# Optimization experiments

Measured on AMD Instinct MI355X. Metric: run time of the kernel, lower is better.

## Reference

```python
import jax, jax.numpy as jnp
import numpy as np

N = 8192
QS = 128
KS = 128
F = 256
EPS = 1e-5     # BatchNorm1d default eps
SLOPE = 0.01   # LeakyReLU default negative_slope


def _leaky(x):
    return jnp.where(x >= 0, x, SLOPE * x)


def _mlp_bn(x, w1, b1, w2, b2, gamma, beta):
    # Sequential(Linear, LeakyReLU, Linear, LeakyReLU) then BatchNorm1d (training mode)
    h = _leaky(x @ w1 + b1)
    h = _leaky(h @ w2 + b2)
    mean = h.mean(axis=0)
    var = h.var(axis=0)  # biased variance, as torch BN uses for normalization
    return gamma * (h - mean) * jax.lax.rsqrt(var + EPS) + beta


def setup_inputs() -> dict:
    key = jax.random.key(0)
    ks = jax.random.split(key, 24)

    def lin_w(k_, fi, fo):
        s = 1.0 / np.sqrt(fi)
        return jax.random.uniform(k_, (fi, fo), minval=-s, maxval=s, dtype=jnp.float32)

    def lin_b(k_, fi, fo):
        s = 1.0 / np.sqrt(fi)
        return jax.random.uniform(k_, (fo,), minval=-s, maxval=s, dtype=jnp.float32)

    A = (jax.random.uniform(ks[0], (N, N)) < 0.004).astype(jnp.float32)
    q = jax.random.normal(ks[1], (N, QS), dtype=jnp.float32)
    k = jax.random.normal(ks[2], (N, KS), dtype=jnp.float32)

    inp = {"A": A, "q": q, "k": k}
    i = 3
    for pre, fi in (("q", QS), ("k", KS), ("v", KS)):
        inp[pre + "_w1"] = lin_w(ks[i], fi, F); i += 1
        inp[pre + "_b1"] = lin_b(ks[i], fi, F); i += 1
        inp[pre + "_w2"] = lin_w(ks[i], F, F); i += 1
        inp[pre + "_b2"] = lin_b(ks[i], F, F); i += 1
        inp[pre + "_gamma"] = jnp.ones((F,), jnp.float32)
        inp[pre + "_beta"] = jnp.zeros((F,), jnp.float32)
    return inp


def reference(A, q, k,
              q_w1, q_b1, q_w2, q_b2, q_gamma, q_beta,
              k_w1, k_b1, k_w2, k_b2, k_gamma, k_beta,
              v_w1, v_b1, v_w2, v_b2, v_gamma, v_beta):
    qe1 = _mlp_bn(q, q_w1, q_b1, q_w2, q_b2, q_gamma, q_beta)   # [N, F]
    ke1 = _mlp_bn(k, k_w1, k_b1, k_w2, k_b2, k_gamma, k_beta)   # [N, F]
    prod = (qe1 @ ke1.T) / jnp.sqrt(jnp.float32(F))             # [N, N]
    # NOTE: faithful to source — mask zeroes scores (not -inf) before softmax
    masked = A * prod
    attn = jax.nn.softmax(masked, axis=1)
    ve1 = _mlp_bn(k, v_w1, v_b1, v_w2, v_b2, v_gamma, v_beta)   # [N, F]
    return attn @ ve1                                            # [N, F]
```

## Files before the change

kernel.cpp:

```cpp
#include <hip/hip_runtime.h>

#define NROWS 8192
#define FDIM 256
#define CAP 128

typedef _Float16 half8_t __attribute__((ext_vector_type(8)));
typedef _Float16 half4_t __attribute__((ext_vector_type(4)));
typedef float floatx4 __attribute__((ext_vector_type(4)));

struct MlpPtrs {
  const float* w1[3]; const float* b1[3];
  const float* w2[3]; const float* b2[3];
  const float* gamma[3]; const float* beta[3];
};

__global__ __launch_bounds__(256) void prep_kernel(
    MlpPtrs p, _Float16* __restrict__ w1p, _Float16* __restrict__ w2p) {
  int task = blockIdx.y;
  int tid = blockIdx.x * 256 + threadIdx.x;
  int m = task % 3;
  bool isw2 = task >= 3;
  int K = isw2 ? 256 : 128;
  if (tid >= K * 256) return;
  const float* src = isw2 ? p.w2[m] : p.w1[m];
  _Float16* dst = isw2 ? (w2p + m * 65536) : (w1p + m * 32768);
  int j = tid & 7, lane = (tid >> 3) & 63, rest = tid >> 9;
  int ktiles = K >> 5;
  int k_tile = rest % ktiles, n_tile = rest / ktiles;
  int kk = k_tile * 32 + (lane >> 4) * 8 + j;
  int nn = n_tile * 16 + (lane & 15);
  dst[tid] = (_Float16)src[kk * 256 + nn];
}

__global__ __launch_bounds__(256) void gemm1_kernel(
    const float* __restrict__ q, const float* __restrict__ k,
    const _Float16* __restrict__ w1p, MlpPtrs p, _Float16* __restrict__ h1) {
  const int mlp = blockIdx.z;
  const float* X = (mlp == 0) ? q : k;
  const _Float16* wp = w1p + mlp * 32768;
  _Float16* out = h1 + (size_t)mlp * (NROWS * FDIM);
  const float* bias = p.b1[mlp];
  int lane = threadIdx.x & 63, wave = threadIdx.x >> 6;
  int lm = lane & 15, lq = lane >> 4;
  int m0 = blockIdx.x * 64 + wave * 16;
  int n0 = blockIdx.y * 64;
  floatx4 acc[4];
  #pragma unroll
  for (int t = 0; t < 4; ++t) acc[t] = (floatx4){0.f, 0.f, 0.f, 0.f};
  const float* ap = X + (size_t)(m0 + lm) * 128 + lq * 8;
  const half8_t* wp8 = (const half8_t*)wp;
  #pragma unroll
  for (int kt = 0; kt < 4; ++kt) {
    floatx4 a0 = *(const floatx4*)(ap + kt * 32);
    floatx4 a1 = *(const floatx4*)(ap + kt * 32 + 4);
    half8_t a = (half8_t){(_Float16)a0[0], (_Float16)a0[1], (_Float16)a0[2], (_Float16)a0[3],
                          (_Float16)a1[0], (_Float16)a1[1], (_Float16)a1[2], (_Float16)a1[3]};
    #pragma unroll
    for (int t = 0; t < 4; ++t) {
      half8_t b = wp8[(((n0 >> 4) + t) * 4 + kt) * 64 + lane];
      acc[t] = __builtin_amdgcn_mfma_f32_16x16x32_f16(a, b, acc[t], 0, 0, 0);
    }
  }
  #pragma unroll
  for (int t = 0; t < 4; ++t) {
    int col = n0 + t * 16 + lm;
    float bb = bias[col];
    #pragma unroll
    for (int r = 0; r < 4; ++r) {
      float v = acc[t][r] + bb;
      v = (v >= 0.f) ? v : 0.01f * v;
      out[(size_t)(m0 + lq * 4 + r) * FDIM + col] = (_Float16)v;
    }
  }
}

__global__ __launch_bounds__(256) void gemm2_kernel(
    const _Float16* __restrict__ h1, const _Float16* __restrict__ w2p,
    MlpPtrs p, _Float16* __restrict__ e1,
    float* __restrict__ colsum, float* __restrict__ colsumsq) {
  const int mlp = blockIdx.z;
  const _Float16* X = h1 + (size_t)mlp * (NROWS * FDIM);
  const _Float16* wp = w2p + mlp * 65536;
  _Float16* out = e1 + (size_t)mlp * (NROWS * FDIM);
  const float* bias = p.b2[mlp];
  int lane = threadIdx.x & 63, wave = threadIdx.x >> 6;
  int lm = lane & 15, lq = lane >> 4;
  int m0 = blockIdx.x * 64 + wave * 16;
  int n0 = blockIdx.y * 64;
  floatx4 acc[4];
  #pragma unroll
  for (int t = 0; t < 4; ++t) acc[t] = (floatx4){0.f, 0.f, 0.f, 0.f};
  const half8_t* ap = (const half8_t*)(X + (size_t)(m0 + lm) * 256 + lq * 8);
  const half8_t* wp8 = (const half8_t*)wp;
  #pragma unroll
  for (int kt = 0; kt < 8; ++kt) {
    half8_t a = ap[kt * 4];
    #pragma unroll
    for (int t = 0; t < 4; ++t) {
      half8_t b = wp8[(((n0 >> 4) + t) * 8 + kt) * 64 + lane];
      acc[t] = __builtin_amdgcn_mfma_f32_16x16x32_f16(a, b, acc[t], 0, 0, 0);
    }
  }
  #pragma unroll
  for (int t = 0; t < 4; ++t) {
    int col = n0 + t * 16 + lm;
    float bb = bias[col];
    float s = 0.f, s2 = 0.f;
    #pragma unroll
    for (int r = 0; r < 4; ++r) {
      float v = acc[t][r] + bb;
      v = (v >= 0.f) ? v : 0.01f * v;
      out[(size_t)(m0 + lq * 4 + r) * FDIM + col] = (_Float16)v;
      s += v; s2 += v * v;
    }
    s  += __shfl_xor(s, 16, 64);  s  += __shfl_xor(s, 32, 64);
    s2 += __shfl_xor(s2, 16, 64); s2 += __shfl_xor(s2, 32, 64);
    if (lq == 0) {
      atomicAdd(&colsum[mlp * FDIM + col], s);
      atomicAdd(&colsumsq[mlp * FDIM + col], s2);
    }
  }
}

__global__ __launch_bounds__(256) void stats_kernel(
    const float* __restrict__ colsum, const float* __restrict__ colsumsq,
    MlpPtrs p, float* __restrict__ scaleA, float* __restrict__ shiftA) {
  int c = threadIdx.x;
  #pragma unroll
  for (int m = 0; m < 3; ++m) {
    float mean = colsum[m * FDIM + c] * (1.f / NROWS);
    float var = colsumsq[m * FDIM + c] * (1.f / NROWS) - mean * mean;
    float sc = p.gamma[m][c] * rsqrtf(var + 1e-5f);
    scaleA[m * FDIM + c] = sc;
    shiftA[m * FDIM + c] = p.beta[m][c] - mean * sc;
  }
}

__global__ __launch_bounds__(256) void attn_kernel(
    const float* __restrict__ A, const _Float16* __restrict__ e1,
    const float* __restrict__ scaleA, const float* __restrict__ shiftA,
    const float* __restrict__ colsum, float* __restrict__ out) {
  const _Float16* qe = e1;
  const _Float16* ke = e1 + (size_t)1 * NROWS * FDIM;
  const _Float16* ve = e1 + (size_t)2 * NROWS * FDIM;
  int lane = threadIdx.x & 63, wave = threadIdx.x >> 6;
  int i = blockIdx.x * 4 + wave;
  __shared__ int sj[4][CAP];
  __shared__ float sw[4][CAP];
  __shared__ int cnt[4];
  if (lane == 0) cnt[wave] = 0;

  const floatx4* row = (const floatx4*)(A + (size_t)i * NROWS);
  for (int b = 0; b < 4; ++b) {
    floatx4 av[8];
    #pragma unroll
    for (int it = 0; it < 8; ++it)
      av[it] = __builtin_nontemporal_load(&row[(b * 8 + it) * 64 + lane]);
    #pragma unroll
    for (int it = 0; it < 8; ++it) {
      int base = ((b * 8 + it) * 64 + lane) * 4;
      int cols[4]; int c = 0;
      if (av[it][0] != 0.f) cols[c++] = base + 0;
      if (av[it][1] != 0.f) cols[c++] = base + 1;
      if (av[it][2] != 0.f) cols[c++] = base + 2;
      if (av[it][3] != 0.f) cols[c++] = base + 3;
      if (c) {
        int pos = atomicAdd(&cnt[wave], c);
        for (int l = 0; l < c; ++l) if (pos + l < CAP) sj[wave][pos + l] = cols[l];
      }
    }
  }
  int nnz = cnt[wave] < CAP ? cnt[wave] : CAP;

  int cl = lane & 15, g = lane >> 4;
  const half8_t* qp = (const half8_t*)(qe + (size_t)i * FDIM + cl * 16);
  half8_t qa = qp[0], qb8 = qp[1];
  const floatx4* sq4 = (const floatx4*)(scaleA + cl * 16);
  const floatx4* hq4 = (const floatx4*)(shiftA + cl * 16);
  const floatx4* sk4 = (const floatx4*)(scaleA + FDIM + cl * 16);
  const floatx4* hk4 = (const floatx4*)(shiftA + FDIM + cl * 16);
  float qk[16]; float qb = 0.f;
  #pragma unroll
  for (int v4 = 0; v4 < 4; ++v4) {
    floatx4 sq = sq4[v4], hq = hq4[v4], sk = sk4[v4], hk = hk4[v4];
    #pragma unroll
    for (int r = 0; r < 4; ++r) {
      int c = v4 * 4 + r;
      float qr = (c < 8) ? (float)qa[c] : (float)qb8[c - 8];
      float qn = qr * sq[r] + hq[r];
      qk[c] = qn * sk[r] * 0.0625f;
      qb += qn * hk[r] * 0.0625f;
    }
  }

  for (int e = g; e < nnz; e += 4) {
    int j = sj[wave][e];
    const half8_t* kp = (const half8_t*)(ke + (size_t)j * FDIM + cl * 16);
    half8_t ka = kp[0], kb = kp[1];
    float s = qb;
    #pragma unroll
    for (int r = 0; r < 8; ++r)
      s += qk[r] * (float)ka[r] + qk[r + 8] * (float)kb[r];
    #pragma unroll
    for (int off = 8; off >= 1; off >>= 1) s += __shfl_xor(s, off, 64);
    if (cl == 0) sw[wave][e] = s;
  }

  float v0 = lane < nnz ? sw[wave][lane] : 0.f;
  float v1 = lane + 64 < nnz ? sw[wave][lane + 64] : 0.f;
  float m = fmaxf(fmaxf(v0, v1), 0.f);
  #pragma unroll
  for (int off = 32; off >= 1; off >>= 1) m = fmaxf(m, __shfl_xor(m, off, 64));
  float em = __expf(-m);
  float w0 = lane < nnz ? __expf(v0 - m) : 0.f;
  float w1 = lane + 64 < nnz ? __expf(v1 - m) : 0.f;
  float ls = w0 + w1;
  #pragma unroll
  for (int off = 32; off >= 1; off >>= 1) ls += __shfl_xor(ls, off, 64);
  if (lane < nnz) sw[wave][lane] = w0 - em;
  if (lane + 64 < nnz) sw[wave][lane + 64] = w1 - em;
  float wsum = ls - (float)nnz * em;
  float inv = 1.f / (ls + (float)(NROWS - nnz) * em);

  floatx4 acc = (floatx4){0.f, 0.f, 0.f, 0.f};
  for (int e = 0; e < nnz; ++e) {
    int j = sj[wave][e];
    float w = sw[wave][e];
    half4_t vv = *(const half4_t*)(ve + (size_t)j * FDIM + lane * 4);
    acc[0] += w * (float)vv[0]; acc[1] += w * (float)vv[1];
    acc[2] += w * (float)vv[2]; acc[3] += w * (float)vv[3];
  }

  floatx4 sv = *(const floatx4*)(scaleA + 2 * FDIM + lane * 4);
  floatx4 sh = *(const floatx4*)(shiftA + 2 * FDIM + lane * 4);
  floatx4 cs = *(const floatx4*)(colsum + 2 * FDIM + lane * 4);
  float bg = wsum + em * (float)NROWS;
  floatx4 o;
  #pragma unroll
  for (int r = 0; r < 4; ++r)
    o[r] = inv * (sv[r] * (acc[r] + em * cs[r]) + sh[r] * bg);
  __builtin_nontemporal_store(o, (floatx4*)(out + (size_t)i * FDIM + lane * 4));
}

extern "C" void kernel_launch(void* const* d_in, const int* in_sizes, int n_in,
                              void* d_out, int out_size, void* d_ws, size_t ws_size,
                              hipStream_t stream) {
  const float* A = (const float*)d_in[0];
  const float* q = (const float*)d_in[1];
  const float* k = (const float*)d_in[2];
  MlpPtrs p;
  for (int m = 0; m < 3; ++m) {
    const int b = 3 + m * 6;
    p.w1[m]    = (const float*)d_in[b + 0];
    p.b1[m]    = (const float*)d_in[b + 1];
    p.w2[m]    = (const float*)d_in[b + 2];
    p.b2[m]    = (const float*)d_in[b + 3];
    p.gamma[m] = (const float*)d_in[b + 4];
    p.beta[m]  = (const float*)d_in[b + 5];
  }
  char* ws = (char*)d_ws;
  const size_t MB = 1024 * 1024;
  _Float16* h1  = (_Float16*)(ws + 0);
  _Float16* e1  = (_Float16*)(ws + 12 * MB);
  _Float16* w1p = (_Float16*)(ws + 24 * MB);
  _Float16* w2p = (_Float16*)(ws + 24 * MB + 192 * 1024);
  float* colsum   = (float*)(ws + 25 * MB);
  float* colsumsq = colsum + 3 * FDIM;
  float* scaleA   = colsumsq + 3 * FDIM;
  float* shiftA   = scaleA + 3 * FDIM;

  (void)hipMemsetAsync(colsum, 0, 2 * 3 * FDIM * sizeof(float), stream);
  prep_kernel<<<dim3(256, 6, 1), 256, 0, stream>>>(p, w1p, w2p);
  gemm1_kernel<<<dim3(128, 4, 3), 256, 0, stream>>>(q, k, w1p, p, h1);
  gemm2_kernel<<<dim3(128, 4, 3), 256, 0, stream>>>(h1, w2p, p, e1, colsum, colsumsq);
  stats_kernel<<<1, 256, 0, stream>>>(colsum, colsumsq, p, scaleA, shiftA);
  attn_kernel<<<NROWS / 4, 256, 0, stream>>>(A, e1, scaleA, shiftA, colsum, (float*)d_out);
}
```

Measured before the change: 456.0 us.

## Cut launches: fold memset and stats into other kernels, widen GEMM tiles

Zeroing of the column-sum buffers moves into the weight-prep kernel, and the single-block stats kernel is removed; each attention block now computes BN scale and shift into shared memory itself. Both MLP GEMM kernels now compute all 256 output columns per block (16 accumulators) instead of 64, so each A row is loaded once and grid size drops fourfold. This removes two launches and their serialization, at the cost of redundant stats work in every attention block, more registers and fewer blocks in the GEMMs.

```diff
diff --git a/kernel.cpp b/kernel.cpp
--- a/kernel.cpp
+++ b/kernel.cpp
@@ -15,9 +15,11 @@
 };
 
 __global__ __launch_bounds__(256) void prep_kernel(
-    MlpPtrs p, _Float16* __restrict__ w1p, _Float16* __restrict__ w2p) {
+    MlpPtrs p, _Float16* __restrict__ w1p, _Float16* __restrict__ w2p,
+    float* __restrict__ colzero) {
   int task = blockIdx.y;
   int tid = blockIdx.x * 256 + threadIdx.x;
+  if (task == 0 && tid < 2 * 3 * FDIM) colzero[tid] = 0.f;
   int m = task % 3;
   bool isw2 = task >= 3;
   int K = isw2 ? 256 : 128;
@@ -43,10 +45,9 @@
   int lane = threadIdx.x & 63, wave = threadIdx.x >> 6;
   int lm = lane & 15, lq = lane >> 4;
   int m0 = blockIdx.x * 64 + wave * 16;
-  int n0 = blockIdx.y * 64;
-  floatx4 acc[4];
-  #pragma unroll
-  for (int t = 0; t < 4; ++t) acc[t] = (floatx4){0.f, 0.f, 0.f, 0.f};
+  floatx4 acc[16];
+  #pragma unroll
+  for (int t = 0; t < 16; ++t) acc[t] = (floatx4){0.f, 0.f, 0.f, 0.f};
   const float* ap = X + (size_t)(m0 + lm) * 128 + lq * 8;
   const half8_t* wp8 = (const half8_t*)wp;
   #pragma unroll
@@ -56,14 +57,14 @@
     half8_t a = (half8_t){(_Float16)a0[0], (_Float16)a0[1], (_Float16)a0[2], (_Float16)a0[3],
                           (_Float16)a1[0], (_Float16)a1[1], (_Float16)a1[2], (_Float16)a1[3]};
     #pragma unroll
-    for (int t = 0; t < 4; ++t) {
-      half8_t b = wp8[(((n0 >> 4) + t) * 4 + kt) * 64 + lane];
+    for (int t = 0; t < 16; ++t) {
+      half8_t b = wp8[(t * 4 + kt) * 64 + lane];
       acc[t] = __builtin_amdgcn_mfma_f32_16x16x32_f16(a, b, acc[t], 0, 0, 0);
     }
   }
   #pragma unroll
-  for (int t = 0; t < 4; ++t) {
-    int col = n0 + t * 16 + lm;
+  for (int t = 0; t < 16; ++t) {
+    int col = t * 16 + lm;
     float bb = bias[col];
     #pragma unroll
     for (int r = 0; r < 4; ++r) {
@@ -86,24 +87,23 @@
   int lane = threadIdx.x & 63, wave = threadIdx.x >> 6;
   int lm = lane & 15, lq = lane >> 4;
   int m0 = blockIdx.x * 64 + wave * 16;
-  int n0 = blockIdx.y * 64;
-  floatx4 acc[4];
-  #pragma unroll
-  for (int t = 0; t < 4; ++t) acc[t] = (floatx4){0.f, 0.f, 0.f, 0.f};
+  floatx4 acc[16];
+  #pragma unroll
+  for (int t = 0; t < 16; ++t) acc[t] = (floatx4){0.f, 0.f, 0.f, 0.f};
   const half8_t* ap = (const half8_t*)(X + (size_t)(m0 + lm) * 256 + lq * 8);
   const half8_t* wp8 = (const half8_t*)wp;
   #pragma unroll
   for (int kt = 0; kt < 8; ++kt) {
     half8_t a = ap[kt * 4];
     #pragma unroll
-    for (int t = 0; t < 4; ++t) {
-      half8_t b = wp8[(((n0 >> 4) + t) * 8 + kt) * 64 + lane];
+    for (int t = 0; t < 16; ++t) {
+      half8_t b = wp8[(t * 8 + kt) * 64 + lane];
       acc[t] = __builtin_amdgcn_mfma_f32_16x16x32_f16(a, b, acc[t], 0, 0, 0);
     }
   }
   #pragma unroll
-  for (int t = 0; t < 4; ++t) {
-    int col = n0 + t * 16 + lm;
+  for (int t = 0; t < 16; ++t) {
+    int col = t * 16 + lm;
     float bb = bias[col];
     float s = 0.f, s2 = 0.f;
     #pragma unroll
@@ -122,33 +122,33 @@
   }
 }
 
-__global__ __launch_bounds__(256) void stats_kernel(
-    const float* __restrict__ colsum, const float* __restrict__ colsumsq,
-    MlpPtrs p, float* __restrict__ scaleA, float* __restrict__ shiftA) {
-  int c = threadIdx.x;
-  #pragma unroll
-  for (int m = 0; m < 3; ++m) {
-    float mean = colsum[m * FDIM + c] * (1.f / NROWS);
-    float var = colsumsq[m * FDIM + c] * (1.f / NROWS) - mean * mean;
-    float sc = p.gamma[m][c] * rsqrtf(var + 1e-5f);
-    scaleA[m * FDIM + c] = sc;
-    shiftA[m * FDIM + c] = p.beta[m][c] - mean * sc;
-  }
-}
-
 __global__ __launch_bounds__(256) void attn_kernel(
     const float* __restrict__ A, const _Float16* __restrict__ e1,
-    const float* __restrict__ scaleA, const float* __restrict__ shiftA,
-    const float* __restrict__ colsum, float* __restrict__ out) {
+    const float* __restrict__ colsum, const float* __restrict__ colsumsq,
+    MlpPtrs p, float* __restrict__ out) {
   const _Float16* qe = e1;
   const _Float16* ke = e1 + (size_t)1 * NROWS * FDIM;
   const _Float16* ve = e1 + (size_t)2 * NROWS * FDIM;
-  int lane = threadIdx.x & 63, wave = threadIdx.x >> 6;
+  int tid = threadIdx.x, lane = tid & 63, wave = tid >> 6;
   int i = blockIdx.x * 4 + wave;
   __shared__ int sj[4][CAP];
   __shared__ float sw[4][CAP];
   __shared__ int cnt[4];
+  __shared__ float ls_scale[3 * FDIM], ls_shift[3 * FDIM];
+
+  {
+    int c = tid;
+    #pragma unroll
+    for (int m = 0; m < 3; ++m) {
+      float mean = colsum[m * FDIM + c] * (1.f / NROWS);
+      float var = colsumsq[m * FDIM + c] * (1.f / NROWS) - mean * mean;
+      float sc = p.gamma[m][c] * rsqrtf(var + 1e-5f);
+      ls_scale[m * FDIM + c] = sc;
+      ls_shift[m * FDIM + c] = p.beta[m][c] - mean * sc;
+    }
+  }
   if (lane == 0) cnt[wave] = 0;
+  __syncthreads();
 
   const floatx4* row = (const floatx4*)(A + (size_t)i * NROWS);
   for (int b = 0; b < 4; ++b) {
@@ -175,10 +175,10 @@
   int cl = lane & 15, g = lane >> 4;
   const half8_t* qp = (const half8_t*)(qe + (size_t)i * FDIM + cl * 16);
   half8_t qa = qp[0], qb8 = qp[1];
-  const floatx4* sq4 = (const floatx4*)(scaleA + cl * 16);
-  const floatx4* hq4 = (const floatx4*)(shiftA + cl * 16);
-  const floatx4* sk4 = (const floatx4*)(scaleA + FDIM + cl * 16);
-  const floatx4* hk4 = (const floatx4*)(shiftA + FDIM + cl * 16);
+  const floatx4* sq4 = (const floatx4*)(ls_scale + cl * 16);
+  const floatx4* hq4 = (const floatx4*)(ls_shift + cl * 16);
+  const floatx4* sk4 = (const floatx4*)(ls_scale + FDIM + cl * 16);
+  const floatx4* hk4 = (const floatx4*)(ls_shift + FDIM + cl * 16);
   float qk[16]; float qb = 0.f;
   #pragma unroll
   for (int v4 = 0; v4 < 4; ++v4) {
@@ -231,8 +231,8 @@
     acc[2] += w * (float)vv[2]; acc[3] += w * (float)vv[3];
   }
 
-  floatx4 sv = *(const floatx4*)(scaleA + 2 * FDIM + lane * 4);
-  floatx4 sh = *(const floatx4*)(shiftA + 2 * FDIM + lane * 4);
+  floatx4 sv = *(const floatx4*)(ls_scale + 2 * FDIM + lane * 4);
+  floatx4 sh = *(const floatx4*)(ls_shift + 2 * FDIM + lane * 4);
   floatx4 cs = *(const floatx4*)(colsum + 2 * FDIM + lane * 4);
   float bg = wsum + em * (float)NROWS;
   floatx4 o;
@@ -266,13 +266,9 @@
   _Float16* w2p = (_Float16*)(ws + 24 * MB + 192 * 1024);
   float* colsum   = (float*)(ws + 25 * MB);
   float* colsumsq = colsum + 3 * FDIM;
-  float* scaleA   = colsumsq + 3 * FDIM;
-  float* shiftA   = scaleA + 3 * FDIM;
-
-  (void)hipMemsetAsync(colsum, 0, 2 * 3 * FDIM * sizeof(float), stream);
-  prep_kernel<<<dim3(256, 6, 1), 256, 0, stream>>>(p, w1p, w2p);
-  gemm1_kernel<<<dim3(128, 4, 3), 256, 0, stream>>>(q, k, w1p, p, h1);
-  gemm2_kernel<<<dim3(128, 4, 3), 256, 0, stream>>>(h1, w2p, p, e1, colsum, colsumsq);
-  stats_kernel<<<1, 256, 0, stream>>>(colsum, colsumsq, p, scaleA, shiftA);
-  attn_kernel<<<NROWS / 4, 256, 0, stream>>>(A, e1, scaleA, shiftA, colsum, (float*)d_out);
-}
+
+  prep_kernel<<<dim3(256, 6, 1), 256, 0, stream>>>(p, w1p, w2p, colsum);
+  gemm1_kernel<<<dim3(128, 1, 3), 256, 0, stream>>>(q, k, w1p, p, h1);
+  gemm2_kernel<<<dim3(128, 1, 3), 256, 0, stream>>>(h1, w2p, p, e1, colsum, colsumsq);
+  attn_kernel<<<NROWS / 4, 256, 0, stream>>>(A, e1, colsum, colsumsq, p, (float*)d_out);
+}
```

New measurement: 487.1 us. 6.8% more time.

## Overlap adjacency scan with MLP GEMMs by folding row compaction into GEMM launches

Applied to the files above, without the earlier changes.

Moves the dense adjacency scan, which reads 256 MB and compacts each row into column indices, out of the attention kernel. The scan now runs as extra blocks inside the two GEMM kernels, half the rows in each, so its memory traffic overlaps the MFMA work. The attention kernel then reads only the compacted index lists. This adds a workspace round-trip for the indices and makes the GEMM launches mix memory-bound and compute-bound blocks.

```diff
diff --git a/kernel.cpp b/kernel.cpp
--- a/kernel.cpp
+++ b/kernel.cpp
@@ -13,6 +13,37 @@
   const float* w2[3]; const float* b2[3];
   const float* gamma[3]; const float* beta[3];
 };
+
+__device__ __forceinline__ void scan_row(
+    int r, int lane, int wave, const float* __restrict__ A,
+    int* __restrict__ colidx, int* __restrict__ rowcnt,
+    int (&sj)[4][CAP], int (&cnt)[4]) {
+  if (lane == 0) cnt[wave] = 0;
+  const floatx4* row = (const floatx4*)(A + (size_t)r * NROWS);
+  for (int b = 0; b < 4; ++b) {
+    floatx4 av[8];
+    #pragma unroll
+    for (int it = 0; it < 8; ++it)
+      av[it] = __builtin_nontemporal_load(&row[(b * 8 + it) * 64 + lane]);
+    #pragma unroll
+    for (int it = 0; it < 8; ++it) {
+      int base = ((b * 8 + it) * 64 + lane) * 4;
+      int cols[4]; int c = 0;
+      if (av[it][0] != 0.f) cols[c++] = base + 0;
+      if (av[it][1] != 0.f) cols[c++] = base + 1;
+      if (av[it][2] != 0.f) cols[c++] = base + 2;
+      if (av[it][3] != 0.f) cols[c++] = base + 3;
+      if (c) {
+        int pos = atomicAdd(&cnt[wave], c);
+        for (int l = 0; l < c; ++l) if (pos + l < CAP) sj[wave][pos + l] = cols[l];
+      }
+    }
+  }
+  int nnz = cnt[wave] < CAP ? cnt[wave] : CAP;
+  if (lane < nnz) colidx[(size_t)r * CAP + lane] = sj[wave][lane];
+  if (lane + 64 < nnz) colidx[(size_t)r * CAP + lane + 64] = sj[wave][lane + 64];
+  if (lane == 0) rowcnt[r] = nnz;
+}
 
 __global__ __launch_bounds__(256) void prep_kernel(
     MlpPtrs p, _Float16* __restrict__ w1p, _Float16* __restrict__ w2p) {
@@ -34,19 +65,28 @@
 
 __global__ __launch_bounds__(256) void gemm1_kernel(
     const float* __restrict__ q, const float* __restrict__ k,
-    const _Float16* __restrict__ w1p, MlpPtrs p, _Float16* __restrict__ h1) {
-  const int mlp = blockIdx.z;
-  const float* X = (mlp == 0) ? q : k;
-  const _Float16* wp = w1p + mlp * 32768;
-  _Float16* out = h1 + (size_t)mlp * (NROWS * FDIM);
-  const float* bias = p.b1[mlp];
+    const _Float16* __restrict__ w1p, MlpPtrs p, _Float16* __restrict__ h1,
+    const float* __restrict__ A, int* __restrict__ colidx, int* __restrict__ rowcnt) {
+  __shared__ int sj[4][CAP];
+  __shared__ int cnt[4];
   int lane = threadIdx.x & 63, wave = threadIdx.x >> 6;
+  int bid = blockIdx.x;
+  if (bid < 1024) {
+    scan_row(bid * 4 + wave, lane, wave, A, colidx, rowcnt, sj, cnt);
+    return;
+  }
+  int t = bid - 1024;
+  int z = t / 512, rem = t % 512, by = rem / 128, bx = rem % 128;
+  const float* X = (z == 0) ? q : k;
+  const _Float16* wp = w1p + z * 32768;
+  _Float16* out = h1 + (size_t)z * (NROWS * FDIM);
+  const float* bias = p.b1[z];
   int lm = lane & 15, lq = lane >> 4;
-  int m0 = blockIdx.x * 64 + wave * 16;
-  int n0 = blockIdx.y * 64;
+  int m0 = bx * 64 + wave * 16;
+  int n0 = by * 64;
   floatx4 acc[4];
   #pragma unroll
-  for (int t = 0; t < 4; ++t) acc[t] = (floatx4){0.f, 0.f, 0.f, 0.f};
+  for (int u = 0; u < 4; ++u) acc[u] = (floatx4){0.f, 0.f, 0.f, 0.f};
   const float* ap = X + (size_t)(m0 + lm) * 128 + lq * 8;
   const half8_t* wp8 = (const half8_t*)wp;
   #pragma unroll
@@ -56,18 +96,18 @@
     half8_t a = (half8_t){(_Float16)a0[0], (_Float16)a0[1], (_Float16)a0[2], (_Float16)a0[3],
                           (_Float16)a1[0], (_Float16)a1[1], (_Float16)a1[2], (_Float16)a1[3]};
     #pragma unroll
-    for (int t = 0; t < 4; ++t) {
-      half8_t b = wp8[(((n0 >> 4) + t) * 4 + kt) * 64 + lane];
-      acc[t] = __builtin_amdgcn_mfma_f32_16x16x32_f16(a, b, acc[t], 0, 0, 0);
-    }
-  }
-  #pragma unroll
-  for (int t = 0; t < 4; ++t) {
-    int col = n0 + t * 16 + lm;
+    for (int u = 0; u < 4; ++u) {
+      half8_t b = wp8[(((n0 >> 4) + u) * 4 + kt) * 64 + lane];
+      acc[u] = __builtin_amdgcn_mfma_f32_16x16x32_f16(a, b, acc[u], 0, 0, 0);
+    }
+  }
+  #pragma unroll
+  for (int u = 0; u < 4; ++u) {
+    int col = n0 + u * 16 + lm;
     float bb = bias[col];
     #pragma unroll
     for (int r = 0; r < 4; ++r) {
-      float v = acc[t][r] + bb;
+      float v = acc[u][r] + bb;
       v = (v >= 0.f) ? v : 0.01f * v;
       out[(size_t)(m0 + lq * 4 + r) * FDIM + col] = (_Float16)v;
     }
@@ -77,38 +117,47 @@
 __global__ __launch_bounds__(256) void gemm2_kernel(
     const _Float16* __restrict__ h1, const _Float16* __restrict__ w2p,
     MlpPtrs p, _Float16* __restrict__ e1,
-    float* __restrict__ colsum, float* __restrict__ colsumsq) {
-  const int mlp = blockIdx.z;
-  const _Float16* X = h1 + (size_t)mlp * (NROWS * FDIM);
-  const _Float16* wp = w2p + mlp * 65536;
-  _Float16* out = e1 + (size_t)mlp * (NROWS * FDIM);
-  const float* bias = p.b2[mlp];
+    float* __restrict__ colsum, float* __restrict__ colsumsq,
+    const float* __restrict__ A, int* __restrict__ colidx, int* __restrict__ rowcnt) {
+  __shared__ int sj[4][CAP];
+  __shared__ int cnt[4];
   int lane = threadIdx.x & 63, wave = threadIdx.x >> 6;
+  int bid = blockIdx.x;
+  if (bid < 1024) {
+    scan_row(4096 + bid * 4 + wave, lane, wave, A, colidx, rowcnt, sj, cnt);
+    return;
+  }
+  int t = bid - 1024;
+  int z = t / 512, rem = t % 512, by = rem / 128, bx = rem % 128;
+  const _Float16* X = h1 + (size_t)z * (NROWS * FDIM);
+  const _Float16* wp = w2p + z * 65536;
+  _Float16* out = e1 + (size_t)z * (NROWS * FDIM);
+  const float* bias = p.b2[z];
   int lm = lane & 15, lq = lane >> 4;
-  int m0 = blockIdx.x * 64 + wave * 16;
-  int n0 = blockIdx.y * 64;
+  int m0 = bx * 64 + wave * 16;
+  int n0 = by * 64;
   floatx4 acc[4];
   #pragma unroll
-  for (int t = 0; t < 4; ++t) acc[t] = (floatx4){0.f, 0.f, 0.f, 0.f};
+  for (int u = 0; u < 4; ++u) acc[u] = (floatx4){0.f, 0.f, 0.f, 0.f};
   const half8_t* ap = (const half8_t*)(X + (size_t)(m0 + lm) * 256 + lq * 8);
   const half8_t* wp8 = (const half8_t*)wp;
   #pragma unroll
   for (int kt = 0; kt < 8; ++kt) {
     half8_t a = ap[kt * 4];
     #pragma unroll
-    for (int t = 0; t < 4; ++t) {
-      half8_t b = wp8[(((n0 >> 4) + t) * 8 + kt) * 64 + lane];
-      acc[t] = __builtin_amdgcn_mfma_f32_16x16x32_f16(a, b, acc[t], 0, 0, 0);
-    }
-  }
-  #pragma unroll
-  for (int t = 0; t < 4; ++t) {
-    int col = n0 + t * 16 + lm;
+    for (int u = 0; u < 4; ++u) {
+      half8_t b = wp8[(((n0 >> 4) + u) * 8 + kt) * 64 + lane];
+      acc[u] = __builtin_amdgcn_mfma_f32_16x16x32_f16(a, b, acc[u], 0, 0, 0);
+    }
+  }
+  #pragma unroll
+  for (int u = 0; u < 4; ++u) {
+    int col = n0 + u * 16 + lm;
     float bb = bias[col];
     float s = 0.f, s2 = 0.f;
     #pragma unroll
     for (int r = 0; r < 4; ++r) {
-      float v = acc[t][r] + bb;
+      float v = acc[u][r] + bb;
       v = (v >= 0.f) ? v : 0.01f * v;
       out[(size_t)(m0 + lq * 4 + r) * FDIM + col] = (_Float16)v;
       s += v; s2 += v * v;
@@ -116,8 +165,8 @@
     s  += __shfl_xor(s, 16, 64);  s  += __shfl_xor(s, 32, 64);
     s2 += __shfl_xor(s2, 16, 64); s2 += __shfl_xor(s2, 32, 64);
     if (lq == 0) {
-      atomicAdd(&colsum[mlp * FDIM + col], s);
-      atomicAdd(&colsumsq[mlp * FDIM + col], s2);
+      atomicAdd(&colsum[z * FDIM + col], s);
+      atomicAdd(&colsumsq[z * FDIM + col], s2);
     }
   }
 }
@@ -137,7 +186,8 @@
 }
 
 __global__ __launch_bounds__(256) void attn_kernel(
-    const float* __restrict__ A, const _Float16* __restrict__ e1,
+    const int* __restrict__ colidx, const int* __restrict__ rowcnt,
+    const _Float16* __restrict__ e1,
     const float* __restrict__ scaleA, const float* __restrict__ shiftA,
     const float* __restrict__ colsum, float* __restrict__ out) {
   const _Float16* qe = e1;
@@ -147,30 +197,10 @@
   int i = blockIdx.x * 4 + wave;
   __shared__ int sj[4][CAP];
   __shared__ float sw[4][CAP];
-  __shared__ int cnt[4];
-  if (lane == 0) cnt[wave] = 0;
-
-  const floatx4* row = (const floatx4*)(A + (size_t)i * NROWS);
-  for (int b = 0; b < 4; ++b) {
-    floatx4 av[8];
-    #pragma unroll
-    for (int it = 0; it < 8; ++it)
-      av[it] = __builtin_nontemporal_load(&row[(b * 8 + it) * 64 + lane]);
-    #pragma unroll
-    for (int it = 0; it < 8; ++it) {
-      int base = ((b * 8 + it) * 64 + lane) * 4;
-      int cols[4]; int c = 0;
-      if (av[it][0] != 0.f) cols[c++] = base + 0;
-      if (av[it][1] != 0.f) cols[c++] = base + 1;
-      if (av[it][2] != 0.f) cols[c++] = base + 2;
-      if (av[it][3] != 0.f) cols[c++] = base + 3;
-      if (c) {
-        int pos = atomicAdd(&cnt[wave], c);
-        for (int l = 0; l < c; ++l) if (pos + l < CAP) sj[wave][pos + l] = cols[l];
-      }
-    }
-  }
-  int nnz = cnt[wave] < CAP ? cnt[wave] : CAP;
+
+  int nnz = rowcnt[i];
+  if (lane < nnz) sj[wave][lane] = colidx[(size_t)i * CAP + lane];
+  if (lane + 64 < nnz) sj[wave][lane + 64] = colidx[(size_t)i * CAP + lane + 64];
 
   int cl = lane & 15, g = lane >> 4;
   const half8_t* qp = (const half8_t*)(qe + (size_t)i * FDIM + cl * 16);
@@ -268,11 +298,13 @@
   float* colsumsq = colsum + 3 * FDIM;
   float* scaleA   = colsumsq + 3 * FDIM;
   float* shiftA   = scaleA + 3 * FDIM;
+  int* colidx = (int*)(ws + 26 * MB);
+  int* rowcnt = (int*)(ws + 30 * MB);
 
   (void)hipMemsetAsync(colsum, 0, 2 * 3 * FDIM * sizeof(float), stream);
   prep_kernel<<<dim3(256, 6, 1), 256, 0, stream>>>(p, w1p, w2p);
-  gemm1_kernel<<<dim3(128, 4, 3), 256, 0, stream>>>(q, k, w1p, p, h1);
-  gemm2_kernel<<<dim3(128, 4, 3), 256, 0, stream>>>(h1, w2p, p, e1, colsum, colsumsq);
+  gemm1_kernel<<<1024 + 1536, 256, 0, stream>>>(q, k, w1p, p, h1, A, colidx, rowcnt);
+  gemm2_kernel<<<1024 + 1536, 256, 0, stream>>>(h1, w2p, p, e1, colsum, colsumsq, A, colidx, rowcnt);
   stats_kernel<<<1, 256, 0, stream>>>(colsum, colsumsq, p, scaleA, shiftA);
-  attn_kernel<<<NROWS / 4, 256, 0, stream>>>(A, e1, scaleA, shiftA, colsum, (float*)d_out);
-}
+  attn_kernel<<<NROWS / 4, 256, 0, stream>>>(colidx, rowcnt, e1, scaleA, shiftA, colsum, (float*)d_out);
+}
```

Measured after the change: 450.9 us. Within noise of the previous version (-1.1%).
